# Kernel optimization log

Measured on AMD Instinct MI355X. Metric: run time of the kernel, lower is better.

## Reference

```python
import jax, jax.numpy as jnp
import numpy as np

LUT_SIZE = 4096
TWO_PI = 2.0 * np.pi


def _lut_sin_cos(theta, sin_table, cos_table):
    # Quantize angle to nearest LUT entry (wrap-around via mod LUT_SIZE)
    idx = jnp.mod(jnp.round(theta * (LUT_SIZE / TWO_PI)), LUT_SIZE).astype(jnp.int32)
    return sin_table[idx], cos_table[idx]


def setup_inputs() -> dict:
    key = jax.random.key(0)
    k_x, k_w, k_o = jax.random.split(key, 3)
    batch, in_features, out_features = 64, 1024, 1024
    num_neurons = 2 * out_features  # default: out_features * 2

    x = jax.random.normal(k_x, (batch, in_features), dtype=jnp.float32)
    W = jax.random.normal(k_w, (num_neurons, in_features), dtype=jnp.float32) * 0.02
    B = jnp.zeros((num_neurons, in_features), dtype=jnp.float32)

    # out_proj: Linear(num_neurons, out_features, bias=False), xavier_uniform gain=0.5
    limit = 0.5 * np.sqrt(6.0 / (num_neurons + out_features))
    out_w = jax.random.uniform(k_o, (out_features, num_neurons), dtype=jnp.float32,
                               minval=-limit, maxval=limit)

    grid = jnp.arange(LUT_SIZE, dtype=jnp.float32) * (TWO_PI / LUT_SIZE)
    sin_table = jnp.sin(grid)
    cos_table = jnp.cos(grid)
    return {"x": x, "W": W, "B": B, "out_w": out_w,
            "sin_table": sin_table, "cos_table": cos_table}


def reference(x, W, B, out_w, sin_table, cos_table):
    # theta: (batch, num_neurons, in_features)
    wavelength = 1.0 + jnp.abs(W)
    theta = x[:, None, :] / wavelength + B
    sin_t, cos_t = _lut_sin_cos(theta, sin_table, cos_table)
    interference = jnp.sum(sin_t + cos_t, axis=-1)  # (batch, num_neurons)
    return interference @ out_w.T  # (batch, out_features)
```

## Files before the change

### kernel.cpp

```cpp
#include <hip/hip_runtime.h>
#include <math.h>

constexpr int BATCH = 64;
constexpr int IN    = 1024;
constexpr int NN    = 2048;
constexpr int OUTF  = 1024;

constexpr float INV2PI = 0.15915494309189535f;
constexpr float SQRT2  = 1.4142135623730951f;


template<int M>
__device__ __forceinline__ void butterfly(float* acc, int lane) {
    const bool hi = (lane & M) != 0;
#pragma unroll
    for (int j = 0; j < M; ++j) {
        const float send = hi ? acc[j] : acc[j + M];
        const float recv = __shfl_xor(send, M, 64);
        acc[j] = (hi ? acc[j + M] : acc[j]) + recv;
    }
    if constexpr (M > 1) butterfly<M / 2>(acc, lane);
}


__global__ __launch_bounds__(512)
__attribute__((amdgpu_waves_per_eu(4, 4)))
void k_interf(const float* __restrict__ x, const float* __restrict__ W,
              const float* __restrict__ B, float* __restrict__ part) {
    __shared__ float xs[2][32 * 256];

    const int tid  = threadIdx.x;
    const int lane = tid & 63;
    const int wv   = __builtin_amdgcn_readfirstlane(tid >> 6);
    const int bid  = blockIdx.x;
    const int h    = bid & 1;
    const int n    = (bid >> 1) * 8 + wv;

    float4 iv2[4], bs2[4];
#pragma unroll
    for (int kc = 0; kc < 4; ++kc) {
        const float4 w4 = *(const float4*)&W[(size_t)n * IN + kc * 256 + 4 * lane];
        const float4 b4 = *(const float4*)&B[(size_t)n * IN + kc * 256 + 4 * lane];
        iv2[kc].x = INV2PI * __builtin_amdgcn_rcpf(1.0f + fabsf(w4.x));
        iv2[kc].y = INV2PI * __builtin_amdgcn_rcpf(1.0f + fabsf(w4.y));
        iv2[kc].z = INV2PI * __builtin_amdgcn_rcpf(1.0f + fabsf(w4.z));
        iv2[kc].w = INV2PI * __builtin_amdgcn_rcpf(1.0f + fabsf(w4.w));
        bs2[kc].x = fmaf(b4.x, INV2PI, 0.125f);
        bs2[kc].y = fmaf(b4.y, INV2PI, 0.125f);
        bs2[kc].z = fmaf(b4.z, INV2PI, 0.125f);
        bs2[kc].w = fmaf(b4.w, INV2PI, 0.125f);
    }

    const float* gx = x + (size_t)(h * 32) * IN;

#define STAGE(KC, P)                                                           \
    {                                                                          \
        _Pragma("unroll")                                                      \
        for (int rr = 0; rr < 4; ++rr) {                                       \
            const int r = wv * 4 + rr;              \
            __builtin_amdgcn_global_load_lds(                                  \
                (const __attribute__((address_space(1))) unsigned int*)        \
                    (gx + (size_t)r * IN + (KC) * 256 + 4 * lane),             \
                (__attribute__((address_space(3))) unsigned int*)              \
                    &xs[(P)][r * 256],                                         \
                16, 0, 0);                                                     \
        }                                                                      \
    }

    float acc[32];
#pragma unroll
    for (int j = 0; j < 32; ++j) acc[j] = 0.0f;

    STAGE(0, 0);
    __syncthreads();

#pragma unroll
    for (int kc = 0; kc < 4; ++kc) {
        const int p = kc & 1;
        if (kc < 3) STAGE(kc + 1, 1 - p);

        const float4 iv = iv2[kc], bs = bs2[kc];
#pragma unroll
        for (int bb = 0; bb < 32; ++bb) {
            const float4 xv = *(const float4*)&xs[p][bb * 256 + 4 * lane];
            const float a0 = fmaf(xv.x, iv.x, bs.x);
            const float a1 = fmaf(xv.y, iv.y, bs.y);
            const float a2 = fmaf(xv.z, iv.z, bs.z);
            const float a3 = fmaf(xv.w, iv.w, bs.w);
            const float t0 = __builtin_amdgcn_sinf(a0);
            const float t1 = __builtin_amdgcn_sinf(a1);
            const float t2 = __builtin_amdgcn_sinf(a2);
            const float t3 = __builtin_amdgcn_sinf(a3);
            acc[bb] += (t0 + t1) + (t2 + t3);
        }
        __syncthreads();
    }
#undef STAGE

#pragma unroll
    for (int j = 0; j < 32; ++j) acc[j] += __shfl_xor(acc[j], 32, 64);
    butterfly<16>(acc, lane);

    if (lane < 32)
        part[(size_t)(h * 32 + lane) * NN + n] = acc[0] * SQRT2;
}


__global__ __launch_bounds__(256)
__attribute__((amdgpu_waves_per_eu(2, 2)))
void k_proj(const float* __restrict__ part, const float* __restrict__ ow,
            float* __restrict__ out) {
    const int tid  = threadIdx.x;
    const int lane = tid & 63;
    const int wv   = __builtin_amdgcn_readfirstlane(tid >> 6);
    const int wid  = blockIdx.x * 4 + wv;
    const int o0   = (wid & 255) * 4;
    const int b0   = (wid >> 8) * 8;

    float4 acc[4][8];
#pragma unroll
    for (int o = 0; o < 4; ++o)
#pragma unroll
        for (int b = 0; b < 8; ++b) acc[o][b] = make_float4(0.f, 0.f, 0.f, 0.f);

    for (int it = 0; it < NN / 256; ++it) {
        const int nb = it * 256 + lane * 4;
        float4 wrow[4], vrow[8];
#pragma unroll
        for (int o = 0; o < 4; ++o)
            wrow[o] = *(const float4*)&ow[(size_t)(o0 + o) * NN + nb];
#pragma unroll
        for (int b = 0; b < 8; ++b)
            vrow[b] = *(const float4*)&part[(size_t)(b0 + b) * NN + nb];
#pragma unroll
        for (int o = 0; o < 4; ++o)
#pragma unroll
            for (int b = 0; b < 8; ++b) {
                acc[o][b].x = fmaf(wrow[o].x, vrow[b].x, acc[o][b].x);
                acc[o][b].y = fmaf(wrow[o].y, vrow[b].y, acc[o][b].y);
                acc[o][b].z = fmaf(wrow[o].z, vrow[b].z, acc[o][b].z);
                acc[o][b].w = fmaf(wrow[o].w, vrow[b].w, acc[o][b].w);
            }
    }

    float accs[32];
#pragma unroll
    for (int o = 0; o < 4; ++o)
#pragma unroll
        for (int b = 0; b < 8; ++b)
            accs[o * 8 + b] = (acc[o][b].x + acc[o][b].y) + (acc[o][b].z + acc[o][b].w);

#pragma unroll
    for (int j = 0; j < 32; ++j) accs[j] += __shfl_xor(accs[j], 32, 64);
    butterfly<16>(accs, lane);

    if (lane < 32)
        out[(size_t)(b0 + (lane & 7)) * OUTF + o0 + (lane >> 3)] = accs[0];
}

extern "C" void kernel_launch(void* const* d_in, const int* in_sizes, int n_in,
                              void* d_out, int out_size, void* d_ws, size_t ws_size,
                              hipStream_t stream) {
    const float* x  = (const float*)d_in[0];
    const float* W  = (const float*)d_in[1];
    const float* B  = (const float*)d_in[2];
    const float* ow = (const float*)d_in[3];
    float* out  = (float*)d_out;
    float* part = (float*)d_ws;

    k_interf<<<dim3(512), dim3(512), 0, stream>>>(x, W, B, part);
    k_proj  <<<dim3(512), dim3(256), 0, stream>>>(part, ow, out);
}
```

Before: 108.3 us.

## Process two neurons per wave and widen projection tiles to 8x8

The interference kernel now gives each wave two neurons instead of one and halves the block size to 256 threads. Each shared-memory x load is reused across both neurons, and W/B chunks are prefetched per k-chunk instead of fully preloaded. The projection kernel computes 8 outputs by 8 batch rows per wave with scalar accumulators and a 64-wide butterfly, using half as many blocks. This cuts LDS reads per sine and reuses loaded projection weights more, at the cost of more registers, fewer waves, and fewer blocks for latency hiding.

```diff
diff --git a/kernel.cpp b/kernel.cpp
--- a/kernel.cpp
+++ b/kernel.cpp
@@ -23,8 +23,8 @@
 }
 
 
-__global__ __launch_bounds__(512)
-__attribute__((amdgpu_waves_per_eu(4, 4)))
+__global__ __launch_bounds__(256)
+__attribute__((amdgpu_waves_per_eu(2, 2)))
 void k_interf(const float* __restrict__ x, const float* __restrict__ W,
               const float* __restrict__ B, float* __restrict__ part) {
     __shared__ float xs[2][32 * 256];
@@ -34,30 +34,15 @@
     const int wv   = __builtin_amdgcn_readfirstlane(tid >> 6);
     const int bid  = blockIdx.x;
     const int h    = bid & 1;
-    const int n    = (bid >> 1) * 8 + wv;
-
-    float4 iv2[4], bs2[4];
-#pragma unroll
-    for (int kc = 0; kc < 4; ++kc) {
-        const float4 w4 = *(const float4*)&W[(size_t)n * IN + kc * 256 + 4 * lane];
-        const float4 b4 = *(const float4*)&B[(size_t)n * IN + kc * 256 + 4 * lane];
-        iv2[kc].x = INV2PI * __builtin_amdgcn_rcpf(1.0f + fabsf(w4.x));
-        iv2[kc].y = INV2PI * __builtin_amdgcn_rcpf(1.0f + fabsf(w4.y));
-        iv2[kc].z = INV2PI * __builtin_amdgcn_rcpf(1.0f + fabsf(w4.z));
-        iv2[kc].w = INV2PI * __builtin_amdgcn_rcpf(1.0f + fabsf(w4.w));
-        bs2[kc].x = fmaf(b4.x, INV2PI, 0.125f);
-        bs2[kc].y = fmaf(b4.y, INV2PI, 0.125f);
-        bs2[kc].z = fmaf(b4.z, INV2PI, 0.125f);
-        bs2[kc].w = fmaf(b4.w, INV2PI, 0.125f);
-    }
+    const int n0   = (bid >> 1) * 8 + wv * 2;
 
     const float* gx = x + (size_t)(h * 32) * IN;
 
 #define STAGE(KC, P)                                                           \
     {                                                                          \
         _Pragma("unroll")                                                      \
-        for (int rr = 0; rr < 4; ++rr) {                                       \
-            const int r = wv * 4 + rr;              \
+        for (int rr = 0; rr < 8; ++rr) {                                       \
+            const int r = wv * 8 + rr;              \
             __builtin_amdgcn_global_load_lds(                                  \
                 (const __attribute__((address_space(1))) unsigned int*)        \
                     (gx + (size_t)r * IN + (KC) * 256 + 4 * lane),             \
@@ -67,42 +52,75 @@
         }                                                                      \
     }
 
-    float acc[32];
+    float4 wc[2], bc[2];
 #pragma unroll
-    for (int j = 0; j < 32; ++j) acc[j] = 0.0f;
+    for (int j = 0; j < 2; ++j) {
+        wc[j] = *(const float4*)&W[(size_t)(n0 + j) * IN + 4 * lane];
+        bc[j] = *(const float4*)&B[(size_t)(n0 + j) * IN + 4 * lane];
+    }
+
+    float acc[64];
+#pragma unroll
+    for (int i = 0; i < 64; ++i) acc[i] = 0.0f;
 
     STAGE(0, 0);
     __syncthreads();
 
-#pragma unroll
+#pragma unroll 1
     for (int kc = 0; kc < 4; ++kc) {
         const int p = kc & 1;
-        if (kc < 3) STAGE(kc + 1, 1 - p);
 
-        const float4 iv = iv2[kc], bs = bs2[kc];
+        float4 wn[2], bn[2];
+        if (kc < 3) {
+#pragma unroll
+            for (int j = 0; j < 2; ++j) {
+                wn[j] = *(const float4*)&W[(size_t)(n0 + j) * IN + (kc + 1) * 256 + 4 * lane];
+                bn[j] = *(const float4*)&B[(size_t)(n0 + j) * IN + (kc + 1) * 256 + 4 * lane];
+            }
+            STAGE(kc + 1, 1 - p);
+        }
+
+        float4 iv[2], bs[2];
+#pragma unroll
+        for (int j = 0; j < 2; ++j) {
+            iv[j].x = INV2PI * __builtin_amdgcn_rcpf(1.0f + fabsf(wc[j].x));
+            iv[j].y = INV2PI * __builtin_amdgcn_rcpf(1.0f + fabsf(wc[j].y));
+            iv[j].z = INV2PI * __builtin_amdgcn_rcpf(1.0f + fabsf(wc[j].z));
+            iv[j].w = INV2PI * __builtin_amdgcn_rcpf(1.0f + fabsf(wc[j].w));
+            bs[j].x = fmaf(bc[j].x, INV2PI, 0.125f);
+            bs[j].y = fmaf(bc[j].y, INV2PI, 0.125f);
+            bs[j].z = fmaf(bc[j].z, INV2PI, 0.125f);
+            bs[j].w = fmaf(bc[j].w, INV2PI, 0.125f);
+        }
+
 #pragma unroll
         for (int bb = 0; bb < 32; ++bb) {
             const float4 xv = *(const float4*)&xs[p][bb * 256 + 4 * lane];
-            const float a0 = fmaf(xv.x, iv.x, bs.x);
-            const float a1 = fmaf(xv.y, iv.y, bs.y);
-            const float a2 = fmaf(xv.z, iv.z, bs.z);
-            const float a3 = fmaf(xv.w, iv.w, bs.w);
-            const float t0 = __builtin_amdgcn_sinf(a0);
-            const float t1 = __builtin_amdgcn_sinf(a1);
-            const float t2 = __builtin_amdgcn_sinf(a2);
-            const float t3 = __builtin_amdgcn_sinf(a3);
-            acc[bb] += (t0 + t1) + (t2 + t3);
+#pragma unroll
+            for (int j = 0; j < 2; ++j) {
+                const float a0 = fmaf(xv.x, iv[j].x, bs[j].x);
+                const float a1 = fmaf(xv.y, iv[j].y, bs[j].y);
+                const float a2 = fmaf(xv.z, iv[j].z, bs[j].z);
+                const float a3 = fmaf(xv.w, iv[j].w, bs[j].w);
+                const float t0 = __builtin_amdgcn_sinf(a0);
+                const float t1 = __builtin_amdgcn_sinf(a1);
+                const float t2 = __builtin_amdgcn_sinf(a2);
+                const float t3 = __builtin_amdgcn_sinf(a3);
+                acc[j * 32 + bb] += (t0 + t1) + (t2 + t3);
+            }
         }
         __syncthreads();
+        if (kc < 3) {
+#pragma unroll
+            for (int j = 0; j < 2; ++j) { wc[j] = wn[j]; bc[j] = bn[j]; }
+        }
     }
 #undef STAGE
 
-#pragma unroll
-    for (int j = 0; j < 32; ++j) acc[j] += __shfl_xor(acc[j], 32, 64);
-    butterfly<16>(acc, lane);
+    butterfly<32>(acc, lane);
 
-    if (lane < 32)
-        part[(size_t)(h * 32 + lane) * NN + n] = acc[0] * SQRT2;
+    const int nst = n0 + (lane >> 5);
+    part[(size_t)(h * 32 + (lane & 31)) * NN + nst] = acc[0] * SQRT2;
 }
 
 
@@ -114,48 +132,39 @@
     const int lane = tid & 63;
     const int wv   = __builtin_amdgcn_readfirstlane(tid >> 6);
     const int wid  = blockIdx.x * 4 + wv;
-    const int o0   = (wid & 255) * 4;
-    const int b0   = (wid >> 8) * 8;
+    const int o0   = (wid & 127) * 8;
+    const int b0   = (wid >> 7) * 8;
 
-    float4 acc[4][8];
+    float acc[64];
 #pragma unroll
-    for (int o = 0; o < 4; ++o)
-#pragma unroll
-        for (int b = 0; b < 8; ++b) acc[o][b] = make_float4(0.f, 0.f, 0.f, 0.f);
+    for (int i = 0; i < 64; ++i) acc[i] = 0.0f;
 
+#pragma unroll 1
     for (int it = 0; it < NN / 256; ++it) {
         const int nb = it * 256 + lane * 4;
-        float4 wrow[4], vrow[8];
+        float4 wrow[8], vrow[8];
 #pragma unroll
-        for (int o = 0; o < 4; ++o)
+        for (int o = 0; o < 8; ++o)
             wrow[o] = *(const float4*)&ow[(size_t)(o0 + o) * NN + nb];
 #pragma unroll
         for (int b = 0; b < 8; ++b)
             vrow[b] = *(const float4*)&part[(size_t)(b0 + b) * NN + nb];
 #pragma unroll
-        for (int o = 0; o < 4; ++o)
+        for (int o = 0; o < 8; ++o)
 #pragma unroll
             for (int b = 0; b < 8; ++b) {
-                acc[o][b].x = fmaf(wrow[o].x, vrow[b].x, acc[o][b].x);
-                acc[o][b].y = fmaf(wrow[o].y, vrow[b].y, acc[o][b].y);
-                acc[o][b].z = fmaf(wrow[o].z, vrow[b].z, acc[o][b].z);
-                acc[o][b].w = fmaf(wrow[o].w, vrow[b].w, acc[o][b].w);
+                float s = acc[o * 8 + b];
+                s = fmaf(wrow[o].x, vrow[b].x, s);
+                s = fmaf(wrow[o].y, vrow[b].y, s);
+                s = fmaf(wrow[o].z, vrow[b].z, s);
+                s = fmaf(wrow[o].w, vrow[b].w, s);
+                acc[o * 8 + b] = s;
             }
     }
 
-    float accs[32];
-#pragma unroll
-    for (int o = 0; o < 4; ++o)
-#pragma unroll
-        for (int b = 0; b < 8; ++b)
-            accs[o * 8 + b] = (acc[o][b].x + acc[o][b].y) + (acc[o][b].z + acc[o][b].w);
+    butterfly<32>(acc, lane);
 
-#pragma unroll
-    for (int j = 0; j < 32; ++j) accs[j] += __shfl_xor(accs[j], 32, 64);
-    butterfly<16>(accs, lane);
-
-    if (lane < 32)
-        out[(size_t)(b0 + (lane & 7)) * OUTF + o0 + (lane >> 3)] = accs[0];
+    out[(size_t)(b0 + (lane & 7)) * OUTF + o0 + (lane >> 3)] = acc[0];
 }
 
 extern "C" void kernel_launch(void* const* d_in, const int* in_sizes, int n_in,
@@ -168,6 +177,6 @@
     float* out  = (float*)d_out;
     float* part = (float*)d_ws;
 
-    k_interf<<<dim3(512), dim3(512), 0, stream>>>(x, W, B, part);
-    k_proj  <<<dim3(512), dim3(256), 0, stream>>>(part, ow, out);
+    k_interf<<<dim3(512), dim3(256), 0, stream>>>(x, W, B, part);
+    k_proj  <<<dim3(256), dim3(256), 0, stream>>>(part, ow, out);
 }
```

Measured after the change: 184.3 us. 70.3% more time.
